# Kernel tuning notes

Hardware: AMD Instinct MI355X
Metric: run time of the kernel (lower is better)

The kernel has to match this reference:

```python
import jax, jax.numpy as jnp
import numpy as np

USER_NUM = 500000
GOODS_NUM = 500000
K = 128
BATCH = 16384


def setup_inputs() -> dict:
    key = jax.random.key(0)
    k1, k2, k3 = jax.random.split(key, 3)
    # Module initializes factors with torch.rand (uniform [0,1))
    user_matrix = jax.random.uniform(k1, (USER_NUM, K), dtype=jnp.float32)
    goods_matrix = jax.random.uniform(k2, (K, GOODS_NUM), dtype=jnp.float32)
    location = jax.random.randint(k3, (BATCH, 2), 0, GOODS_NUM, dtype=jnp.int64)
    return {"user_matrix": user_matrix, "goods_matrix": goods_matrix, "location": location}


def reference(user_matrix, goods_matrix, location):
    # Vectorized form of the per-pair loop: for each row i,
    # out[i] = dot(user_matrix[location[i,0], :], goods_matrix[:, location[i,1]])
    u = user_matrix[location[:, 0], :]        # [B, K] row gather
    g = goods_matrix[:, location[:, 1]].T     # [B, K] column gather
    out = jnp.sum(u * g, axis=-1, keepdims=True)  # [B, 1]
    return out
```

## Files before the change

kernel.cpp:

```cpp
#include <hip/hip_runtime.h>


#define KDIM 128
#define GOODS_NUM 500000
#define OPW 4

__global__ __launch_bounds__(256) void als_gather_dot4(
    const float* __restrict__ user,
    const float* __restrict__ goods,
    const int* __restrict__ loc,
    float* __restrict__ out,
    int batch)
{
    const int gtid = blockIdx.x * blockDim.x + threadIdx.x;
    const int wave = gtid >> 6;
    const int lane = threadIdx.x & 63;
    const int base = wave * OPW;
    if (base >= batch) return;

    const int r = lane * 2;

    float2 uv[OPW];
    float g0[OPW], g1[OPW];
    #pragma unroll
    for (int j = 0; j < OPW; ++j) {
        const int b = base + j;
        const int urow = loc[b * 2 + 0];
        const int gcol = loc[b * 2 + 1];
        uv[j] = *reinterpret_cast<const float2*>(
            user + (size_t)urow * KDIM + (size_t)r);
        g0[j] = goods[(size_t)r       * GOODS_NUM + (size_t)gcol];
        g1[j] = goods[(size_t)(r + 1) * GOODS_NUM + (size_t)gcol];
    }

    #pragma unroll
    for (int j = 0; j < OPW; ++j) {
        float s = uv[j].x * g0[j] + uv[j].y * g1[j];
        #pragma unroll
        for (int off = 32; off >= 1; off >>= 1)
            s += __shfl_xor(s, off, 64);
        if (lane == 0) out[base + j] = s;
    }
}

extern "C" void kernel_launch(void* const* d_in, const int* in_sizes, int n_in,
                              void* d_out, int out_size, void* d_ws, size_t ws_size,
                              hipStream_t stream)
{
    const float* user  = (const float*)d_in[0];
    const float* goods = (const float*)d_in[1];
    const int*   loc   = (const int*)d_in[2];
    float* out = (float*)d_out;

    const int batch = out_size;
    const int waves = (batch + OPW - 1) / OPW;
    const int threads = 256;
    const int blocks = (waves * 64 + threads - 1) / threads;
    als_gather_dot4<<<blocks, threads, 0, stream>>>(user, goods, loc, out, batch);
}
```

Baseline: 47.96 us.

## Bucket-sort batch by goods column and swizzle blocks across XCDs

Adds a single-block counting sort that groups batch entries into buckets of 32 goods columns, so that waves processing neighbouring columns share cache lines in the strided column gather of the goods matrix. The gather kernel then reads through the permutation and scatters results back, and block indices are remapped so contiguous sorted chunks land on the same XCD and share its L2. The cost is an extra serial single-block kernel launch with shared-memory atomics over the whole batch, plus one more level of indirection per pair. With 16384 random columns over 500000, the 32-column buckets hold about one entry each, so little reuse may result.

```diff
diff --git a/kernel.cpp b/kernel.cpp
--- a/kernel.cpp
+++ b/kernel.cpp
@@ -3,17 +3,71 @@
 
 #define KDIM 128
 #define GOODS_NUM 500000
+#define NBUCKET 15625
 #define OPW 4
 
-__global__ __launch_bounds__(256) void als_gather_dot4(
+__global__ __launch_bounds__(1024) void als_bucket_sort(
+    const int* __restrict__ loc, int* __restrict__ perm, int batch)
+{
+    __shared__ int hist[NBUCKET];
+    __shared__ int wsum[16];
+    const int t = threadIdx.x;
+    const int lane = t & 63, wid = t >> 6;
+
+    for (int i = t; i < NBUCKET; i += 1024) hist[i] = 0;
+    __syncthreads();
+
+    for (int i = t; i < batch; i += 1024)
+        atomicAdd(&hist[loc[2 * i + 1] >> 5], 1);
+    __syncthreads();
+
+    const int CH = 16;
+    int local_excl[CH];
+    int sum = 0;
+    const int base = t * CH;
+    #pragma unroll
+    for (int c = 0; c < CH; ++c) {
+        int idx = base + c;
+        int v = (idx < NBUCKET) ? hist[idx] : 0;
+        local_excl[c] = sum;
+        sum += v;
+    }
+    int x = sum;
+    #pragma unroll
+    for (int off = 1; off < 64; off <<= 1) {
+        int y = __shfl_up(x, off, 64);
+        if (lane >= off) x += y;
+    }
+    if (lane == 63) wsum[wid] = x;
+    __syncthreads();
+    int woff = 0;
+    for (int w = 0; w < wid; ++w) woff += wsum[w];
+    const int chunk_excl = woff + x - sum;
+    #pragma unroll
+    for (int c = 0; c < CH; ++c) {
+        int idx = base + c;
+        if (idx < NBUCKET) hist[idx] = chunk_excl + local_excl[c];
+    }
+    __syncthreads();
+
+    for (int i = t; i < batch; i += 1024) {
+        int b = loc[2 * i + 1] >> 5;
+        int pos = atomicAdd(&hist[b], 1);
+        perm[pos] = i;
+    }
+}
+
+__global__ __launch_bounds__(256) void als_gather_dot_perm(
     const float* __restrict__ user,
     const float* __restrict__ goods,
     const int* __restrict__ loc,
+    const int* __restrict__ perm,
     float* __restrict__ out,
-    int batch)
+    int batch, int chunk_per_xcd)
 {
-    const int gtid = blockIdx.x * blockDim.x + threadIdx.x;
-    const int wave = gtid >> 6;
+    int h = blockIdx.x;
+    int swz = (chunk_per_xcd > 0) ? (h & 7) * chunk_per_xcd + (h >> 3) : h;
+    const int wave = swz * (256 / 64) + (threadIdx.x >> 6);
     const int lane = threadIdx.x & 63;
     const int base = wave * OPW;
     if (base >= batch) return;
@@ -22,11 +76,13 @@
 
     float2 uv[OPW];
     float g0[OPW], g1[OPW];
+    int bidx[OPW];
     #pragma unroll
     for (int j = 0; j < OPW; ++j) {
-        const int b = base + j;
-        const int urow = loc[b * 2 + 0];
-        const int gcol = loc[b * 2 + 1];
+        const int b = perm[base + j];
+        bidx[j] = b;
+        const int urow = loc[2 * b + 0];
+        const int gcol = loc[2 * b + 1];
         uv[j] = *reinterpret_cast<const float2*>(
             user + (size_t)urow * KDIM + (size_t)r);
         g0[j] = goods[(size_t)r       * GOODS_NUM + (size_t)gcol];
@@ -39,7 +95,7 @@
         #pragma unroll
         for (int off = 32; off >= 1; off >>= 1)
             s += __shfl_xor(s, off, 64);
-        if (lane == 0) out[base + j] = s;
+        if (lane == 0) out[bidx[j]] = s;
     }
 }
 
@@ -51,10 +107,15 @@
     const float* goods = (const float*)d_in[1];
     const int*   loc   = (const int*)d_in[2];
     float* out = (float*)d_out;
+    int*   perm = (int*)d_ws;
 
     const int batch = out_size;
+
+    als_bucket_sort<<<1, 1024, 0, stream>>>(loc, perm, batch);
+
     const int waves = (batch + OPW - 1) / OPW;
-    const int threads = 256;
-    const int blocks = (waves * 64 + threads - 1) / threads;
-    als_gather_dot4<<<blocks, threads, 0, stream>>>(user, goods, loc, out, batch);
+    const int blocks = (waves * 64 + 255) / 256;
+    const int chunk = (blocks % 8 == 0) ? blocks / 8 : 0;
+    als_gather_dot_perm<<<blocks, 256, 0, stream>>>(
+        user, goods, loc, perm, out, batch, chunk);
 }
```

Result: slower. 59.25 us (+23.5%).
